# Kernel tuning notes

Hardware: AMD Instinct MI355X
Metric: run time of the kernel (lower is better)

Reference implementation:

```python
import jax, jax.numpy as jnp
import numpy as np

NBINS = 256
HMIN, HMAX = 0.0, 255.0

def _histc(x, nbins=NBINS, lo=HMIN, hi=HMAX):
    # Faithful torch.histc: bin width (hi-lo)/nbins; values outside [lo,hi] ignored;
    # values == hi fall into the last bin. Returns float counts.
    xf = x.reshape(-1)
    width = (hi - lo) / nbins
    idx = jnp.floor((xf - lo) / width).astype(jnp.int32)
    idx = jnp.minimum(idx, nbins - 1)            # x == hi -> last bin
    in_range = (xf >= lo) & (xf <= hi)
    idx = jnp.where(in_range, idx, nbins)        # out-of-range -> dropped bucket
    hist = jnp.zeros(nbins + 1, dtype=x.dtype).at[idx].add(1.0)
    return hist[:nbins]

def setup_inputs() -> dict:
    key = jax.random.key(0)
    # intensity image with values in [0, 255]
    x = jax.random.uniform(key, (8192, 4096), dtype=jnp.float32) * 255.0
    return {"batchsize": 16, "input": x}

def reference(batchsize, input):
    hist = _histc(input)                          # [256] float counts
    # Original loop recomputes the same histc each iter and does
    # count += hist[0] (scalar broadcast into all 256 slots).
    count = jnp.zeros(NBINS, dtype=hist.dtype) + jnp.asarray(batchsize, hist.dtype) * hist[0]
    return (hist, count)
```

## Files before the change

### kernel.cpp

```cpp
#include <hip/hip_runtime.h>

#define NBINS 256
#define BLOCK 256
#define CNT_DW (64 * BLOCK)
#define BIN_SCALE (256.0f / 255.0f)
#define TARGET_G 1024
#define MAX_PER_THREAD 240

__global__ void zero_out(float* __restrict__ out) {
    const int i = blockIdx.x * blockDim.x + threadIdx.x;
    if (i < 2 * NBINS) out[i] = 0.0f;
}

__device__ __forceinline__ void classify(float v, int t, int& dw, unsigned& inc) {
    int idx = (int)(v * BIN_SCALE);
    idx = idx < 255 ? idx : 255;
    const bool ok = (v >= 0.0f) && (v <= 255.0f);
    dw = ok ? ((((unsigned)idx >> 2) << 8) + t) : t;
    inc = ok ? (1u << ((idx & 3) << 3)) : 0u;
}

__global__ __launch_bounds__(BLOCK) void hist_kernel(const float* __restrict__ x,
                                                     unsigned int* __restrict__ partial,
                                                     float* __restrict__ out,
                                                     int n, int G, int use_ws) {
    __shared__ unsigned int cnt[CNT_DW];
    const int t = threadIdx.x;

    {
        uint4* z4 = (uint4*)cnt;
#pragma unroll
        for (int i = 0; i < CNT_DW / 4 / BLOCK; ++i)
            z4[t + i * BLOCK] = make_uint4(0u, 0u, 0u, 0u);
    }
    __syncthreads();

    const int n4 = n >> 2;
    const float4* __restrict__ x4 = (const float4*)x;
    const int S = G * BLOCK;
    const int i0 = blockIdx.x * BLOCK + t;
    const int K = (i0 < n4) ? ((n4 - i0 + S - 1) / S) : 0;

    int pd0 = t, pd1 = t, pd2 = t, pd3 = t;
    unsigned ps0 = 0, ps1 = 0, ps2 = 0, ps3 = 0;
    unsigned po0 = 0, po1 = 0, po2 = 0, po3 = 0;
    bool have_p = false;

    auto process = [&](const float4& v) {
        int d0, d1, d2, d3; unsigned s0, s1, s2, s3;
        classify(v.x, t, d0, s0);
        classify(v.y, t, d1, s1);
        classify(v.z, t, d2, s2);
        classify(v.w, t, d3, s3);
        unsigned w0 = po0 + ps0;
        unsigned w1 = po1 + ps1 + (pd1 == pd0 ? ps0 : 0u);
        unsigned w2 = po2 + ps2 + (pd2 == pd0 ? ps0 : 0u) + (pd2 == pd1 ? ps1 : 0u);
        unsigned w3 = po3 + ps3 + (pd3 == pd0 ? ps0 : 0u) + (pd3 == pd1 ? ps1 : 0u)
                                + (pd3 == pd2 ? ps2 : 0u);
        cnt[pd0] = w0; cnt[pd1] = w1; cnt[pd2] = w2; cnt[pd3] = w3;
        po0 = cnt[d0]; po1 = cnt[d1]; po2 = cnt[d2]; po3 = cnt[d3];
        pd0 = d0; pd1 = d1; pd2 = d2; pd3 = d3;
        ps0 = s0; ps1 = s1; ps2 = s2; ps3 = s3;
    };

    if (K > 0) {
        have_p = true;
        float4 A = x4[i0];
        process(A);

        if (K >= 3) {
            float4 B = x4[i0 + S];
            float4 C = x4[i0 + 2 * S];
            int k = 1;
            for (; k + 1 < K; k += 2) {
                float4 nb = x4[i0 + (k + 2 < K ? (k + 2) : 0) * S];
                process(B);
                float4 nc = x4[i0 + (k + 3 < K ? (k + 3) : 0) * S];
                process(C);
                B = nb; C = nc;
            }
            if (k < K) process(B);
        } else {
            for (int k = 1; k < K; ++k) {
                float4 B = x4[i0 + k * S];
                process(B);
            }
        }
    }
    if (have_p) {
        unsigned w0 = po0 + ps0;
        unsigned w1 = po1 + ps1 + (pd1 == pd0 ? ps0 : 0u);
        unsigned w2 = po2 + ps2 + (pd2 == pd0 ? ps0 : 0u) + (pd2 == pd1 ? ps1 : 0u);
        unsigned w3 = po3 + ps3 + (pd3 == pd0 ? ps0 : 0u) + (pd3 == pd1 ? ps1 : 0u)
                                + (pd3 == pd2 ? ps2 : 0u);
        cnt[pd0] = w0; cnt[pd1] = w1; cnt[pd2] = w2; cnt[pd3] = w3;
    }

    for (int j = (n4 << 2) + i0; j < n; j += S) {
        int d; unsigned s;
        classify(x[j], t, d, s);
        cnt[d] += s;
    }
    __syncthreads();

    const int q = t >> 2;
    const int p = t & 3;
    unsigned accA = 0, accB = 0;
#pragma unroll 16
    for (int j = 0; j < 64; ++j) {
        unsigned u = cnt[(q << 8) + (p << 6) + ((j + t) & 63)];
        accA += u & 0x00FF00FFu;
        accB += (u >> 8) & 0x00FF00FFu;
    }
    accA += __shfl_xor(accA, 1, 64);
    accA += __shfl_xor(accA, 2, 64);
    accB += __shfl_xor(accB, 1, 64);
    accB += __shfl_xor(accB, 2, 64);

    if (p == 0) {
        const unsigned b0 = accA & 0xFFFFu, b2 = accA >> 16;
        const unsigned b1 = accB & 0xFFFFu, b3 = accB >> 16;
        if (use_ws) {
            ((uint4*)(partial + (size_t)blockIdx.x * NBINS))[q] = make_uint4(b0, b1, b2, b3);
        } else {
            if (b0) atomicAdd(&out[4 * q + 0], (float)b0);
            if (b1) atomicAdd(&out[4 * q + 1], (float)b1);
            if (b2) atomicAdd(&out[4 * q + 2], (float)b2);
            if (b3) atomicAdd(&out[4 * q + 3], (float)b3);
        }
    }
}

__global__ __launch_bounds__(NBINS) void reduce_kernel(const unsigned int* __restrict__ partial,
                                                       float* __restrict__ out,
                                                       int G, int slice) {
    const int bin = threadIdx.x;
    const int g0 = blockIdx.x * slice;
    const int g1 = (g0 + slice < G) ? (g0 + slice) : G;
    unsigned s = 0;
    for (int g = g0; g < g1; ++g)
        s += partial[(size_t)g * NBINS + bin];
    if (s) atomicAdd(&out[bin], (float)s);
}

__global__ void count_kernel(const void* __restrict__ bs_raw,
                             float* __restrict__ out) {
    const int as_int = *(const int*)bs_raw;
    float bs;
    if (as_int >= 1 && as_int < (1 << 20)) {
        bs = (float)as_int;
    } else {
        bs = *(const float*)bs_raw;
    }
    out[NBINS + threadIdx.x] = bs * out[0];
}

extern "C" void kernel_launch(void* const* d_in, const int* in_sizes, int n_in,
                              void* d_out, int out_size, void* d_ws, size_t ws_size,
                              hipStream_t stream) {
    const void* bs_ptr;
    const float* x;
    int n;
    if (n_in >= 2 && in_sizes[0] == 1) {
        bs_ptr = d_in[0];
        x = (const float*)d_in[1];
        n = in_sizes[1];
    } else {
        bs_ptr = d_in[1];
        x = (const float*)d_in[0];
        n = in_sizes[0];
    }

    float* out = (float*)d_out;
    unsigned int* partial = (unsigned int*)d_ws;

    long Gmin = ((long)n + (long)BLOCK * MAX_PER_THREAD - 1) / ((long)BLOCK * MAX_PER_THREAD);
    int G = (int)(Gmin > TARGET_G ? Gmin : TARGET_G);
    if (G < 1) G = 1;

    const size_t ws_need = (size_t)G * NBINS * sizeof(unsigned int);
    const int use_ws = (ws_size >= ws_need) ? 1 : 0;

    zero_out<<<2, 256, 0, stream>>>(out);
    hist_kernel<<<G, BLOCK, 0, stream>>>(x, partial, out, n, G, use_ws);
    if (use_ws) {
        const int slice = (G + NBINS - 1) / NBINS;
        reduce_kernel<<<NBINS, NBINS, 0, stream>>>(partial, out, G, slice);
    }
    count_kernel<<<1, NBINS, 0, stream>>>(bs_ptr, out);
}
```

Before: 205.1 us.

## Replace per-thread packed byte counters with per-wave shared-memory atomic histograms

Drops the per-thread private 8-bit packed LDS counter scheme, with its manual read-modify-write pipelining and collision fixups, in favor of one 256-bin histogram per wavefront updated with LDS atomicAdd. The grid is fixed at 2048 blocks with occupancy hint 8, and the block reduction becomes a simple sum of four wave histograms. This cuts LDS footprint and instruction count, but LDS atomics can serialize when lanes in a wave hit the same bin, which uniform data makes fairly common across 64 lanes and 256 bins.

```diff
diff --git a/kernel.cpp b/kernel.cpp
--- a/kernel.cpp
+++ b/kernel.cpp
@@ -2,132 +2,56 @@
 
 #define NBINS 256
 #define BLOCK 256
-#define CNT_DW (64 * BLOCK)
+#define WAVES (BLOCK / 64)
 #define BIN_SCALE (256.0f / 255.0f)
-#define TARGET_G 1024
-#define MAX_PER_THREAD 240
+#define GRID 2048
 
 __global__ void zero_out(float* __restrict__ out) {
     const int i = blockIdx.x * blockDim.x + threadIdx.x;
     if (i < 2 * NBINS) out[i] = 0.0f;
 }
 
-__device__ __forceinline__ void classify(float v, int t, int& dw, unsigned& inc) {
+__device__ __forceinline__ void bump(float v, unsigned* __restrict__ hw) {
     int idx = (int)(v * BIN_SCALE);
     idx = idx < 255 ? idx : 255;
-    const bool ok = (v >= 0.0f) && (v <= 255.0f);
-    dw = ok ? ((((unsigned)idx >> 2) << 8) + t) : t;
-    inc = ok ? (1u << ((idx & 3) << 3)) : 0u;
+    if (v >= 0.0f && v <= 255.0f)
+        atomicAdd(&hw[idx], 1u);
 }
 
-__global__ __launch_bounds__(BLOCK) void hist_kernel(const float* __restrict__ x,
-                                                     unsigned int* __restrict__ partial,
-                                                     float* __restrict__ out,
-                                                     int n, int G, int use_ws) {
-    __shared__ unsigned int cnt[CNT_DW];
+__global__ __launch_bounds__(BLOCK, 8) void hist_kernel(const float* __restrict__ x,
+                                                        unsigned int* __restrict__ partial,
+                                                        float* __restrict__ out,
+                                                        int n, int G, int use_ws) {
+    __shared__ unsigned int h[WAVES][NBINS];
     const int t = threadIdx.x;
+    unsigned* __restrict__ hw = h[t >> 6];
 
-    {
-        uint4* z4 = (uint4*)cnt;
 #pragma unroll
-        for (int i = 0; i < CNT_DW / 4 / BLOCK; ++i)
-            z4[t + i * BLOCK] = make_uint4(0u, 0u, 0u, 0u);
-    }
+    for (int i = t; i < WAVES * NBINS; i += BLOCK) ((unsigned*)h)[i] = 0u;
     __syncthreads();
 
     const int n4 = n >> 2;
     const float4* __restrict__ x4 = (const float4*)x;
     const int S = G * BLOCK;
     const int i0 = blockIdx.x * BLOCK + t;
-    const int K = (i0 < n4) ? ((n4 - i0 + S - 1) / S) : 0;
 
-    int pd0 = t, pd1 = t, pd2 = t, pd3 = t;
-    unsigned ps0 = 0, ps1 = 0, ps2 = 0, ps3 = 0;
-    unsigned po0 = 0, po1 = 0, po2 = 0, po3 = 0;
-    bool have_p = false;
+    for (int i = i0; i < n4; i += S) {
+        const float4 v = x4[i];
+        bump(v.x, hw);
+        bump(v.y, hw);
+        bump(v.z, hw);
+        bump(v.w, hw);
+    }
+    for (int j = (n4 << 2) + i0; j < n; j += S)
+        bump(x[j], hw);
 
-    auto process = [&](const float4& v) {
-        int d0, d1, d2, d3; unsigned s0, s1, s2, s3;
-        classify(v.x, t, d0, s0);
-        classify(v.y, t, d1, s1);
-        classify(v.z, t, d2, s2);
-        classify(v.w, t, d3, s3);
-        unsigned w0 = po0 + ps0;
-        unsigned w1 = po1 + ps1 + (pd1 == pd0 ? ps0 : 0u);
-        unsigned w2 = po2 + ps2 + (pd2 == pd0 ? ps0 : 0u) + (pd2 == pd1 ? ps1 : 0u);
-        unsigned w3 = po3 + ps3 + (pd3 == pd0 ? ps0 : 0u) + (pd3 == pd1 ? ps1 : 0u)
-                                + (pd3 == pd2 ? ps2 : 0u);
-        cnt[pd0] = w0; cnt[pd1] = w1; cnt[pd2] = w2; cnt[pd3] = w3;
-        po0 = cnt[d0]; po1 = cnt[d1]; po2 = cnt[d2]; po3 = cnt[d3];
-        pd0 = d0; pd1 = d1; pd2 = d2; pd3 = d3;
-        ps0 = s0; ps1 = s1; ps2 = s2; ps3 = s3;
-    };
-
-    if (K > 0) {
-        have_p = true;
-        float4 A = x4[i0];
-        process(A);
-
-        if (K >= 3) {
-            float4 B = x4[i0 + S];
-            float4 C = x4[i0 + 2 * S];
-            int k = 1;
-            for (; k + 1 < K; k += 2) {
-                float4 nb = x4[i0 + (k + 2 < K ? (k + 2) : 0) * S];
-                process(B);
-                float4 nc = x4[i0 + (k + 3 < K ? (k + 3) : 0) * S];
-                process(C);
-                B = nb; C = nc;
-            }
-            if (k < K) process(B);
-        } else {
-            for (int k = 1; k < K; ++k) {
-                float4 B = x4[i0 + k * S];
-                process(B);
-            }
-        }
-    }
-    if (have_p) {
-        unsigned w0 = po0 + ps0;
-        unsigned w1 = po1 + ps1 + (pd1 == pd0 ? ps0 : 0u);
-        unsigned w2 = po2 + ps2 + (pd2 == pd0 ? ps0 : 0u) + (pd2 == pd1 ? ps1 : 0u);
-        unsigned w3 = po3 + ps3 + (pd3 == pd0 ? ps0 : 0u) + (pd3 == pd1 ? ps1 : 0u)
-                                + (pd3 == pd2 ? ps2 : 0u);
-        cnt[pd0] = w0; cnt[pd1] = w1; cnt[pd2] = w2; cnt[pd3] = w3;
-    }
-
-    for (int j = (n4 << 2) + i0; j < n; j += S) {
-        int d; unsigned s;
-        classify(x[j], t, d, s);
-        cnt[d] += s;
-    }
     __syncthreads();
 
-    const int q = t >> 2;
-    const int p = t & 3;
-    unsigned accA = 0, accB = 0;
-#pragma unroll 16
-    for (int j = 0; j < 64; ++j) {
-        unsigned u = cnt[(q << 8) + (p << 6) + ((j + t) & 63)];
-        accA += u & 0x00FF00FFu;
-        accB += (u >> 8) & 0x00FF00FFu;
-    }
-    accA += __shfl_xor(accA, 1, 64);
-    accA += __shfl_xor(accA, 2, 64);
-    accB += __shfl_xor(accB, 1, 64);
-    accB += __shfl_xor(accB, 2, 64);
-
-    if (p == 0) {
-        const unsigned b0 = accA & 0xFFFFu, b2 = accA >> 16;
-        const unsigned b1 = accB & 0xFFFFu, b3 = accB >> 16;
-        if (use_ws) {
-            ((uint4*)(partial + (size_t)blockIdx.x * NBINS))[q] = make_uint4(b0, b1, b2, b3);
-        } else {
-            if (b0) atomicAdd(&out[4 * q + 0], (float)b0);
-            if (b1) atomicAdd(&out[4 * q + 1], (float)b1);
-            if (b2) atomicAdd(&out[4 * q + 2], (float)b2);
-            if (b3) atomicAdd(&out[4 * q + 3], (float)b3);
-        }
+    unsigned s = h[0][t] + h[1][t] + h[2][t] + h[3][t];
+    if (use_ws) {
+        partial[(size_t)blockIdx.x * NBINS + t] = s;
+    } else if (s) {
+        atomicAdd(&out[t], (float)s);
     }
 }
 
@@ -174,10 +98,7 @@
     float* out = (float*)d_out;
     unsigned int* partial = (unsigned int*)d_ws;
 
-    long Gmin = ((long)n + (long)BLOCK * MAX_PER_THREAD - 1) / ((long)BLOCK * MAX_PER_THREAD);
-    int G = (int)(Gmin > TARGET_G ? Gmin : TARGET_G);
-    if (G < 1) G = 1;
-
+    const int G = GRID;
     const size_t ws_need = (size_t)G * NBINS * sizeof(unsigned int);
     const int use_ws = (ws_size >= ws_need) ? 1 : 0;
 
```

Result: faster. 196.9 us (-4.0%).
